# Performance work log

Measured on AMD Instinct MI355X. Metric: run time of the kernel, lower is better.

The kernel has to match this reference:

```python
import jax, jax.numpy as jnp
import numpy as np

N_NODES = 100000
N_EDGES = 1600000
D_IN = 128
D_HID = 128
D_OUT = 1


def setup_inputs() -> dict:
    key = jax.random.key(0)
    ks = jax.random.split(key, 8)
    x = jax.random.normal(ks[0], (N_NODES, D_IN), dtype=jnp.float32)
    edge_index = jax.random.randint(ks[1], (2, N_EDGES), 0, N_NODES, dtype=jnp.int64)
    s1 = 1.0 / np.sqrt(D_IN)
    s2 = 1.0 / np.sqrt(D_HID)
    W1 = jax.random.uniform(ks[2], (D_IN, D_HID), jnp.float32, -s1, s1)
    b1 = jnp.zeros((D_HID,), jnp.float32)
    W2 = jax.random.uniform(ks[3], (D_HID, D_HID), jnp.float32, -s2, s2)
    b2 = jnp.zeros((D_HID,), jnp.float32)
    Wl = jax.random.uniform(ks[4], (D_HID, D_OUT), jnp.float32, -s2, s2)
    bl = jax.random.uniform(ks[5], (D_OUT,), jnp.float32, -s2, s2)
    return {"x": x, "edge_index": edge_index, "W1": W1, "b1": b1,
            "W2": W2, "b2": b2, "Wl": Wl, "bl": bl}


def _gcn_norm(edge_index, num_nodes):
    # Add self-loops, compute symmetric normalization 1/sqrt(deg_s * deg_d).
    loops = jnp.arange(num_nodes, dtype=edge_index.dtype)
    src = jnp.concatenate([edge_index[0], loops])
    dst = jnp.concatenate([edge_index[1], loops])
    deg = jax.ops.segment_sum(jnp.ones_like(dst, dtype=jnp.float32), dst,
                              num_segments=num_nodes)
    dinv = jnp.where(deg > 0, jax.lax.rsqrt(deg), 0.0)
    norm = dinv[src] * dinv[dst]  # [E + N]
    return src, dst, norm


def _gcn_conv(h, W, b, src, dst, norm, num_nodes):
    h = h @ W                                  # [N, d_out]
    msg = h[src] * norm[:, None]               # [E+N, d_out] gather
    out = jax.ops.segment_sum(msg, dst, num_segments=num_nodes)  # scatter-add
    return out + b


def reference(x, edge_index, W1, b1, W2, b2, Wl, bl):
    num_nodes = x.shape[0]
    src, dst, norm = _gcn_norm(edge_index, num_nodes)
    h = jax.nn.relu(_gcn_conv(x, W1, b1, src, dst, norm, num_nodes))
    # dropout is identity in eval mode
    h = jax.nn.relu(_gcn_conv(h, W2, b2, src, dst, norm, num_nodes))
    return h @ Wl + bl
```

## Files before the change

kernel.cpp:

```cpp
#include <hip/hip_runtime.h>

#define DHID 128
#define BCAP 10240
#define PCHUNK 4096
#define XS_LD 136

typedef _Float16 h4 __attribute__((ext_vector_type(4)));
typedef _Float16 h8 __attribute__((ext_vector_type(8)));
typedef _Float16 f16x8 __attribute__((ext_vector_type(8)));
typedef float    f32x4 __attribute__((ext_vector_type(4)));

__global__ __launch_bounds__(256) void k_partition(const int* __restrict__ ei, int E, int nbuck,
                                                   int* __restrict__ bucket_cursor,
                                                   unsigned* __restrict__ packed) {
    __shared__ unsigned sdata[PCHUNK];
    __shared__ int lcnt[256], lbase[256], loff[256], lcur[256], sscan[256];
    int t = threadIdx.x;
    int e0 = blockIdx.x * PCHUNK;
    lcnt[t] = 0;
    __syncthreads();

    int sreg[16], dreg[16];
#pragma unroll
    for (int k = 0; k < 16; ++k) {
        int e = e0 + t + k * 256;
        if (e < E) {
            sreg[k] = ei[e];
            dreg[k] = ei[E + e];
        } else {
            dreg[k] = -1;
        }
    }

#pragma unroll
    for (int k = 0; k < 16; ++k)
        if (dreg[k] >= 0) atomicAdd(&lcnt[dreg[k] >> 9], 1);
    __syncthreads();

    int c = lcnt[t];
    sscan[t] = c;
    __syncthreads();
    for (int off = 1; off < 256; off <<= 1) {
        int v = (t >= off) ? sscan[t - off] : 0;
        __syncthreads();
        sscan[t] += v;
        __syncthreads();
    }
    loff[t] = sscan[t] - c;
    if (t < nbuck && c > 0) lbase[t] = atomicAdd(&bucket_cursor[t], c);
    lcur[t] = sscan[t] - c;
    __syncthreads();

#pragma unroll
    for (int k = 0; k < 16; ++k) {
        if (dreg[k] >= 0) {
            int b = dreg[k] >> 9;
            int pos = atomicAdd(&lcur[b], 1);
            sdata[pos] = ((unsigned)(dreg[k] & 511) << 17) | (unsigned)sreg[k];
        }
    }
    __syncthreads();

    int wid = t >> 6, lane = t & 63;
    for (int b = wid; b < nbuck; b += 4) {
        int cb = lcnt[b];
        if (cb == 0) continue;
        int gbase = b * BCAP + lbase[b];
        int sbase = loff[b];
        for (int k = lane; k < cb; k += 64) packed[gbase + k] = sdata[sbase + k];
    }
}

__global__ void k_bscan(const int* __restrict__ bcur, int* __restrict__ bbase,
                        int* __restrict__ row_ptr, int nbuck, int N, int E) {
    __shared__ int s[256];
    int t = threadIdx.x;
    int c = (t < nbuck) ? bcur[t] : 0;
    s[t] = c;
    __syncthreads();
    for (int off = 1; off < 256; off <<= 1) {
        int v = (t >= off) ? s[t - off] : 0;
        __syncthreads();
        s[t] += v;
        __syncthreads();
    }
    if (t <= nbuck) bbase[t] = (t == 0) ? 0 : s[t - 1];
    if (t == 0) row_ptr[N] = E;
}

__global__ __launch_bounds__(256) void k_p2b(const unsigned* __restrict__ packed,
                                             const int* __restrict__ bucket_cursor,
                                             const int* __restrict__ bbase,
                                             int* __restrict__ row_ptr,
                                             float* __restrict__ dinv,
                                             int* __restrict__ csr, int N) {
    __shared__ int c512[512], cur512[512], sscan[256];
    int t = threadIdx.x, b = blockIdx.x;
    c512[t] = 0; c512[t + 256] = 0;
    __syncthreads();
    int m = bucket_cursor[b];
    const unsigned* pb = packed + (size_t)b * BCAP;
    for (int i = t; i < m; i += 256) atomicAdd(&c512[pb[i] >> 17], 1);
    __syncthreads();
    int v0 = c512[2 * t], v1 = c512[2 * t + 1];
    int ps = v0 + v1;
    sscan[t] = ps;
    __syncthreads();
    for (int off = 1; off < 256; off <<= 1) {
        int v = (t >= off) ? sscan[t - off] : 0;
        __syncthreads();
        sscan[t] += v;
        __syncthreads();
    }
    int excl = sscan[t] - ps;
    cur512[2 * t] = excl;
    cur512[2 * t + 1] = excl + v0;

    int rbase = bbase[b];
    int n0 = (b << 9) + 2 * t;
    if (n0 < N) {
        row_ptr[n0] = rbase + excl;
        dinv[n0] = rsqrtf((float)(v0 + 1));
    }
    if (n0 + 1 < N) {
        row_ptr[n0 + 1] = rbase + excl + v0;
        dinv[n0 + 1] = rsqrtf((float)(v1 + 1));
    }
    __syncthreads();

    for (int i = t; i < m; i += 256) {
        unsigned p = pb[i];
        int dl = p >> 17;
        int src = (int)(p & 0x1FFFFu);
        int pos = atomicAdd(&cur512[dl], 1);
        csr[rbase + pos] = src;
    }
}

template <typename TIN>
__global__ __launch_bounds__(256) void k_gemm_mfma(const TIN* __restrict__ X,
                                                   const float* __restrict__ W,
                                                   const float* __restrict__ dinv,
                                                   _Float16* __restrict__ Th, int N) {
    __shared__ _Float16 Xs[64 * XS_LD];
    int t = threadIdx.x;
    int w = t >> 6;
    int l = t & 63;
    int l16 = l & 15;
    int lq = l >> 4;

    f16x8 afrag[2][4];
#pragma unroll
    for (int ct = 0; ct < 2; ++ct) {
        int c = w * 32 + ct * 16 + l16;
#pragma unroll
        for (int kb = 0; kb < 4; ++kb) {
            f16x8 a;
#pragma unroll
            for (int j = 0; j < 8; ++j)
                a[j] = (_Float16)W[(kb * 32 + lq * 8 + j) * DHID + c];
            afrag[ct][kb] = a;
        }
    }

    int rs = t >> 2;
    int cs = (t & 3) * 32;

    int r0 = blockIdx.x * 64;
    {
        int rg = r0 + rs; if (rg > N - 1) rg = N - 1;
        _Float16* sp = Xs + rs * XS_LD + cs;
        if constexpr (sizeof(TIN) == 4) {
            const float* xp = (const float*)X + (size_t)rg * DHID + cs;
#pragma unroll
            for (int k = 0; k < 4; ++k) {
                float4 a = *(const float4*)(xp + k * 8);
                float4 b = *(const float4*)(xp + k * 8 + 4);
                h8 v;
                v[0] = (_Float16)a.x; v[1] = (_Float16)a.y;
                v[2] = (_Float16)a.z; v[3] = (_Float16)a.w;
                v[4] = (_Float16)b.x; v[5] = (_Float16)b.y;
                v[6] = (_Float16)b.z; v[7] = (_Float16)b.w;
                *(h8*)(sp + k * 8) = v;
            }
        } else {
            const _Float16* xp = (const _Float16*)X + (size_t)rg * DHID + cs;
#pragma unroll
            for (int k = 0; k < 4; ++k)
                *(h8*)(sp + k * 8) = *(const h8*)(xp + k * 8);
        }
    }
    __syncthreads();

    f32x4 acc[4][2];
#pragma unroll
    for (int rt = 0; rt < 4; ++rt)
#pragma unroll
        for (int ct = 0; ct < 2; ++ct) acc[rt][ct] = (f32x4){0.f, 0.f, 0.f, 0.f};

#pragma unroll
    for (int rt = 0; rt < 4; ++rt) {
        const _Float16* bp = Xs + (rt * 16 + l16) * XS_LD + lq * 8;
#pragma unroll
        for (int kb = 0; kb < 4; ++kb) {
            f16x8 b = *(const f16x8*)(bp + kb * 32);
            acc[rt][0] = __builtin_amdgcn_mfma_f32_16x16x32_f16(afrag[0][kb], b, acc[rt][0], 0, 0, 0);
            acc[rt][1] = __builtin_amdgcn_mfma_f32_16x16x32_f16(afrag[1][kb], b, acc[rt][1], 0, 0, 0);
        }
    }

#pragma unroll
    for (int rt = 0; rt < 4; ++rt) {
        int r = r0 + rt * 16 + l16;
        if (r < N) {
            float s = dinv[r];
#pragma unroll
            for (int ct = 0; ct < 2; ++ct) {
                h4 v;
#pragma unroll
                for (int j = 0; j < 4; ++j) v[j] = (_Float16)(acc[rt][ct][j] * s);
                *(h4*)(Th + (size_t)r * DHID + w * 32 + ct * 16 + lq * 4) = v;
            }
        }
    }
}

template <int FINAL>
__global__ __launch_bounds__(256) void k_agg(const _Float16* __restrict__ Th,
                                             const int* __restrict__ row_ptr,
                                             const int* __restrict__ csr_src,
                                             const float* __restrict__ dinv,
                                             const float* __restrict__ bias,
                                             void* __restrict__ outp,
                                             const float* __restrict__ Wl,
                                             const float* __restrict__ bl, int N) {
    int node = blockIdx.x * 16 + (threadIdx.x >> 4);
    int sl = threadIdx.x & 15;
    if (node >= N) return;

    int e = row_ptr[node];
    int end = row_ptr[node + 1];
    const h8* Tl = (const h8*)Th + sl;

    float acc[8];
#pragma unroll
    for (int c = 0; c < 8; ++c) acc[c] = 0.f;

    for (; e + 4 <= end; e += 4) {
        int s0 = csr_src[e];
        int s1 = csr_src[e + 1];
        int s2 = csr_src[e + 2];
        int s3 = csr_src[e + 3];
        h8 v0 = Tl[(size_t)s0 * 16];
        h8 v1 = Tl[(size_t)s1 * 16];
        h8 v2 = Tl[(size_t)s2 * 16];
        h8 v3 = Tl[(size_t)s3 * 16];
#pragma unroll
        for (int c = 0; c < 8; ++c)
            acc[c] += ((float)v0[c] + (float)v1[c]) + ((float)v2[c] + (float)v3[c]);
    }
    for (; e < end; ++e) {
        int s0 = csr_src[e];
        h8 va = Tl[(size_t)s0 * 16];
#pragma unroll
        for (int c = 0; c < 8; ++c) acc[c] += (float)va[c];
    }

    {
        h8 tv = Tl[(size_t)node * 16];
#pragma unroll
        for (int c = 0; c < 8; ++c) acc[c] += (float)tv[c];
    }

    float dn = dinv[node];
    const float* bp = bias + sl * 8;
    float4 b0 = *(const float4*)bp;
    float4 b1 = *(const float4*)(bp + 4);
    float r[8];
    r[0] = fmaxf(fmaf(dn, acc[0], b0.x), 0.f);
    r[1] = fmaxf(fmaf(dn, acc[1], b0.y), 0.f);
    r[2] = fmaxf(fmaf(dn, acc[2], b0.z), 0.f);
    r[3] = fmaxf(fmaf(dn, acc[3], b0.w), 0.f);
    r[4] = fmaxf(fmaf(dn, acc[4], b1.x), 0.f);
    r[5] = fmaxf(fmaf(dn, acc[5], b1.y), 0.f);
    r[6] = fmaxf(fmaf(dn, acc[6], b1.z), 0.f);
    r[7] = fmaxf(fmaf(dn, acc[7], b1.w), 0.f);

    if (FINAL == 0) {
        h8 v;
#pragma unroll
        for (int c = 0; c < 8; ++c) v[c] = (_Float16)r[c];
        *(h8*)((_Float16*)outp + (size_t)node * DHID + sl * 8) = v;
    } else {
        const float* wp = Wl + sl * 8;
        float4 w0 = *(const float4*)wp;
        float4 w1 = *(const float4*)(wp + 4);
        float p = r[0] * w0.x + r[1] * w0.y + r[2] * w0.z + r[3] * w0.w +
                  r[4] * w1.x + r[5] * w1.y + r[6] * w1.z + r[7] * w1.w;
#pragma unroll
        for (int off = 8; off > 0; off >>= 1) p += __shfl_down(p, off, 16);
        if (sl == 0) ((float*)outp)[node] = p + bl[0];
    }
}

extern "C" void kernel_launch(void* const* d_in, const int* in_sizes, int n_in,
                              void* d_out, int out_size, void* d_ws, size_t ws_size,
                              hipStream_t stream) {
    const float* x  = (const float*)d_in[0];
    const int*   ei = (const int*)d_in[1];
    const float* W1 = (const float*)d_in[2];
    const float* b1 = (const float*)d_in[3];
    const float* W2 = (const float*)d_in[4];
    const float* b2 = (const float*)d_in[5];
    const float* Wl = (const float*)d_in[6];
    const float* bl = (const float*)d_in[7];
    float* out = (float*)d_out;

    int N = in_sizes[0] / DHID;
    int E = in_sizes[1] / 2;
    int nbuck = (N + 511) / 512;
    int nRB = (N + 63) / 64;

    char* ws = (char*)d_ws;
    size_t off = 0;
    auto alloc = [&](size_t bytes) -> void* {
        void* p = ws + off;
        off += (bytes + 255) & ~(size_t)255;
        return p;
    };
    float*    dinv     = (float*)alloc((size_t)N * 4);
    int*      row_ptr  = (int*)alloc((size_t)(N + 1) * 4);
    int*      bcur     = (int*)alloc((size_t)nbuck * 4);
    int*      bbase    = (int*)alloc((size_t)(nbuck + 1) * 4);
    int*      csr      = (int*)alloc((size_t)E * 4);
    unsigned* packed   = (unsigned*)alloc((size_t)nbuck * BCAP * 4);
    _Float16* Th       = (_Float16*)alloc((size_t)N * DHID * 2);
    _Float16* H        = (_Float16*)alloc((size_t)N * DHID * 2);

    (void)hipMemsetAsync(bcur, 0, (size_t)nbuck * 4, stream);
    k_partition<<<(E + PCHUNK - 1) / PCHUNK, 256, 0, stream>>>(ei, E, nbuck, bcur, packed);
    k_bscan<<<1, 256, 0, stream>>>(bcur, bbase, row_ptr, nbuck, N, E);
    k_p2b<<<nbuck, 256, 0, stream>>>(packed, bcur, bbase, row_ptr, dinv, csr, N);

    k_gemm_mfma<float><<<nRB, 256, 0, stream>>>(x, W1, dinv, Th, N);
    k_agg<0><<<(N + 15) / 16, 256, 0, stream>>>(Th, row_ptr, csr, dinv, b1, H, nullptr, nullptr, N);

    k_gemm_mfma<_Float16><<<nRB, 256, 0, stream>>>(H, W2, dinv, Th, N);
    k_agg<1><<<(N + 15) / 16, 256, 0, stream>>>(Th, row_ptr, csr, dinv, b2, out, Wl, bl, N);
}
```

Measured before the change: 214.1 us.

## Fuse GEMM1 with edge partition and fuse layer-1 aggregation with GEMM2

Merges the first GEMM and the edge partitioning into one launch by splitting blocks between the two roles. This lets GEMM1 run before the degrees are known, so the per-source dinv scale moves into the aggregation as a gather of dinv[src]. The bucket scan is folded into k_p2b, where every block redoes it. A spare block in that kernel transposes W2 to fp16. Layer-1 aggregation is fused with the GEMM2 MFMA through a 16-row shared tile, which removes the H round trip and two launches, at the cost of an extra dinv gather per edge and a low-row-count MFMA per block.

Measured after the change: 210.4 us. No clear change (-1.8%).

```diff
diff --git a/kernel.cpp b/kernel.cpp
--- a/kernel.cpp
+++ b/kernel.cpp
@@ -4,19 +4,106 @@
 #define BCAP 10240
 #define PCHUNK 4096
 #define XS_LD 136
+#define SMEM_BYTES 21504
 
 typedef _Float16 h4 __attribute__((ext_vector_type(4)));
 typedef _Float16 h8 __attribute__((ext_vector_type(8)));
-typedef _Float16 f16x8 __attribute__((ext_vector_type(8)));
 typedef float    f32x4 __attribute__((ext_vector_type(4)));
 
-__global__ __launch_bounds__(256) void k_partition(const int* __restrict__ ei, int E, int nbuck,
-                                                   int* __restrict__ bucket_cursor,
-                                                   unsigned* __restrict__ packed) {
-    __shared__ unsigned sdata[PCHUNK];
-    __shared__ int lcnt[256], lbase[256], loff[256], lcur[256], sscan[256];
+__device__ inline void hoist_afrag_f16(const _Float16* __restrict__ Wt, int w, int l16, int lq,
+                                       h8 afrag[2][4]) {
+#pragma unroll
+    for (int ct = 0; ct < 2; ++ct) {
+        int c = w * 32 + ct * 16 + l16;
+#pragma unroll
+        for (int kb = 0; kb < 4; ++kb)
+            afrag[ct][kb] = *(const h8*)(Wt + (size_t)c * DHID + kb * 32 + lq * 8);
+    }
+}
+
+__device__ inline void gemm1_body(char* smem, const float* __restrict__ X,
+                                  const float* __restrict__ W,
+                                  _Float16* __restrict__ Th, int N, int blk) {
+    _Float16* Xs = (_Float16*)smem;
     int t = threadIdx.x;
-    int e0 = blockIdx.x * PCHUNK;
+    int w = t >> 6, l = t & 63, l16 = l & 15, lq = l >> 4;
+
+    h8 afrag[2][4];
+#pragma unroll
+    for (int ct = 0; ct < 2; ++ct) {
+        int c = w * 32 + ct * 16 + l16;
+#pragma unroll
+        for (int kb = 0; kb < 4; ++kb) {
+            h8 a;
+#pragma unroll
+            for (int j = 0; j < 8; ++j)
+                a[j] = (_Float16)W[(kb * 32 + lq * 8 + j) * DHID + c];
+            afrag[ct][kb] = a;
+        }
+    }
+
+    int rs = t >> 2, cs = (t & 3) * 32;
+    int r0 = blk * 64;
+    {
+        int rg = r0 + rs; if (rg > N - 1) rg = N - 1;
+        _Float16* sp = Xs + rs * XS_LD + cs;
+        const float* xp = X + (size_t)rg * DHID + cs;
+#pragma unroll
+        for (int k = 0; k < 4; ++k) {
+            float4 a = *(const float4*)(xp + k * 8);
+            float4 b = *(const float4*)(xp + k * 8 + 4);
+            h8 v;
+            v[0] = (_Float16)a.x; v[1] = (_Float16)a.y;
+            v[2] = (_Float16)a.z; v[3] = (_Float16)a.w;
+            v[4] = (_Float16)b.x; v[5] = (_Float16)b.y;
+            v[6] = (_Float16)b.z; v[7] = (_Float16)b.w;
+            *(h8*)(sp + k * 8) = v;
+        }
+    }
+    __syncthreads();
+
+    f32x4 acc[4][2];
+#pragma unroll
+    for (int rt = 0; rt < 4; ++rt)
+#pragma unroll
+        for (int ct = 0; ct < 2; ++ct) acc[rt][ct] = (f32x4){0.f, 0.f, 0.f, 0.f};
+
+#pragma unroll
+    for (int rt = 0; rt < 4; ++rt) {
+        const _Float16* bp = Xs + (rt * 16 + l16) * XS_LD + lq * 8;
+#pragma unroll
+        for (int kb = 0; kb < 4; ++kb) {
+            h8 b = *(const h8*)(bp + kb * 32);
+            acc[rt][0] = __builtin_amdgcn_mfma_f32_16x16x32_f16(afrag[0][kb], b, acc[rt][0], 0, 0, 0);
+            acc[rt][1] = __builtin_amdgcn_mfma_f32_16x16x32_f16(afrag[1][kb], b, acc[rt][1], 0, 0, 0);
+        }
+    }
+
+#pragma unroll
+    for (int rt = 0; rt < 4; ++rt) {
+        int r = r0 + rt * 16 + l16;
+        if (r < N) {
+#pragma unroll
+            for (int ct = 0; ct < 2; ++ct) {
+                h4 v;
+#pragma unroll
+                for (int j = 0; j < 4; ++j) v[j] = (_Float16)acc[rt][ct][j];
+                *(h4*)(Th + (size_t)r * DHID + w * 32 + ct * 16 + lq * 4) = v;
+            }
+        }
+    }
+}
+
+__device__ inline void partition_body(char* smem, const int* __restrict__ ei, int E, int nbuck,
+                                      int* __restrict__ bcur, unsigned* __restrict__ packed, int blk) {
+    unsigned* sdata = (unsigned*)smem;
+    int* lcnt  = (int*)(smem + 16384);
+    int* lbase = (int*)(smem + 17408);
+    int* loff  = (int*)(smem + 18432);
+    int* lcur  = (int*)(smem + 19456);
+    int* sscan = (int*)(smem + 20480);
+    int t = threadIdx.x;
+    int e0 = blk * PCHUNK;
     lcnt[t] = 0;
     __syncthreads();
 
@@ -24,12 +111,8 @@
 #pragma unroll
     for (int k = 0; k < 16; ++k) {
         int e = e0 + t + k * 256;
-        if (e < E) {
-            sreg[k] = ei[e];
-            dreg[k] = ei[E + e];
-        } else {
-            dreg[k] = -1;
-        }
+        if (e < E) { sreg[k] = ei[e]; dreg[k] = ei[E + e]; }
+        else dreg[k] = -1;
     }
 
 #pragma unroll
@@ -47,7 +130,7 @@
         __syncthreads();
     }
     loff[t] = sscan[t] - c;
-    if (t < nbuck && c > 0) lbase[t] = atomicAdd(&bucket_cursor[t], c);
+    if (t < nbuck && c > 0) lbase[t] = atomicAdd(&bcur[t], c);
     lcur[t] = sscan[t] - c;
     __syncthreads();
 
@@ -71,34 +154,52 @@
     }
 }
 
-__global__ void k_bscan(const int* __restrict__ bcur, int* __restrict__ bbase,
-                        int* __restrict__ row_ptr, int nbuck, int N, int E) {
-    __shared__ int s[256];
-    int t = threadIdx.x;
-    int c = (t < nbuck) ? bcur[t] : 0;
-    s[t] = c;
-    __syncthreads();
-    for (int off = 1; off < 256; off <<= 1) {
-        int v = (t >= off) ? s[t - off] : 0;
-        __syncthreads();
-        s[t] += v;
-        __syncthreads();
-    }
-    if (t <= nbuck) bbase[t] = (t == 0) ? 0 : s[t - 1];
-    if (t == 0) row_ptr[N] = E;
+__global__ __launch_bounds__(256) void k_front(const float* __restrict__ X,
+                                               const float* __restrict__ W1,
+                                               _Float16* __restrict__ Th, int N, int nRB,
+                                               const int* __restrict__ ei, int E, int nbuck,
+                                               int* __restrict__ bcur, unsigned* __restrict__ packed) {
+    __shared__ __align__(16) char smem[SMEM_BYTES];
+    if ((int)blockIdx.x < nRB)
+        gemm1_body(smem, X, W1, Th, N, blockIdx.x);
+    else
+        partition_body(smem, ei, E, nbuck, bcur, packed, blockIdx.x - nRB);
 }
 
 __global__ __launch_bounds__(256) void k_p2b(const unsigned* __restrict__ packed,
-                                             const int* __restrict__ bucket_cursor,
-                                             const int* __restrict__ bbase,
+                                             const int* __restrict__ bcur,
                                              int* __restrict__ row_ptr,
                                              float* __restrict__ dinv,
-                                             int* __restrict__ csr, int N) {
-    __shared__ int c512[512], cur512[512], sscan[256];
+                                             int* __restrict__ csr,
+                                             const float* __restrict__ W2,
+                                             _Float16* __restrict__ W2t,
+                                             int nbuck, int N, int E) {
     int t = threadIdx.x, b = blockIdx.x;
+    if (b == nbuck) {
+        int c = t & 127, k0 = (t >> 7) * 64;
+#pragma unroll
+        for (int kb = 0; kb < 8; ++kb) {
+            h8 v;
+#pragma unroll
+            for (int j = 0; j < 8; ++j)
+                v[j] = (_Float16)W2[(size_t)(k0 + kb * 8 + j) * DHID + c];
+            *(h8*)(W2t + (size_t)c * DHID + k0 + kb * 8) = v;
+        }
+        return;
+    }
+
+    __shared__ int c512[512], cur512[512], sscan[256], sbk[256];
+    sbk[t] = (t < nbuck) ? bcur[t] : 0;
     c512[t] = 0; c512[t + 256] = 0;
     __syncthreads();
-    int m = bucket_cursor[b];
+    for (int off = 1; off < 256; off <<= 1) {
+        int v = (t >= off) ? sbk[t - off] : 0;
+        __syncthreads();
+        sbk[t] += v;
+        __syncthreads();
+    }
+    int rbase = (b > 0) ? sbk[b - 1] : 0;
+    int m = bcur[b];
     const unsigned* pb = packed + (size_t)b * BCAP;
     for (int i = t; i < m; i += 256) atomicAdd(&c512[pb[i] >> 17], 1);
     __syncthreads();
@@ -116,7 +217,6 @@
     cur512[2 * t] = excl;
     cur512[2 * t + 1] = excl + v0;
 
-    int rbase = bbase[b];
     int n0 = (b << 9) + 2 * t;
     if (n0 < N) {
         row_ptr[n0] = rbase + excl;
@@ -126,6 +226,7 @@
         row_ptr[n0 + 1] = rbase + excl + v0;
         dinv[n0 + 1] = rsqrtf((float)(v1 + 1));
     }
+    if (b == 0 && t == 0) row_ptr[N] = E;
     __syncthreads();
 
     for (int i = t; i < m; i += 256) {
@@ -137,109 +238,26 @@
     }
 }
 
-template <typename TIN>
-__global__ __launch_bounds__(256) void k_gemm_mfma(const TIN* __restrict__ X,
-                                                   const float* __restrict__ W,
-                                                   const float* __restrict__ dinv,
-                                                   _Float16* __restrict__ Th, int N) {
-    __shared__ _Float16 Xs[64 * XS_LD];
-    int t = threadIdx.x;
-    int w = t >> 6;
-    int l = t & 63;
-    int l16 = l & 15;
-    int lq = l >> 4;
-
-    f16x8 afrag[2][4];
-#pragma unroll
-    for (int ct = 0; ct < 2; ++ct) {
-        int c = w * 32 + ct * 16 + l16;
-#pragma unroll
-        for (int kb = 0; kb < 4; ++kb) {
-            f16x8 a;
-#pragma unroll
-            for (int j = 0; j < 8; ++j)
-                a[j] = (_Float16)W[(kb * 32 + lq * 8 + j) * DHID + c];
-            afrag[ct][kb] = a;
-        }
-    }
-
-    int rs = t >> 2;
-    int cs = (t & 3) * 32;
-
-    int r0 = blockIdx.x * 64;
-    {
-        int rg = r0 + rs; if (rg > N - 1) rg = N - 1;
-        _Float16* sp = Xs + rs * XS_LD + cs;
-        if constexpr (sizeof(TIN) == 4) {
-            const float* xp = (const float*)X + (size_t)rg * DHID + cs;
-#pragma unroll
-            for (int k = 0; k < 4; ++k) {
-                float4 a = *(const float4*)(xp + k * 8);
-                float4 b = *(const float4*)(xp + k * 8 + 4);
-                h8 v;
-                v[0] = (_Float16)a.x; v[1] = (_Float16)a.y;
-                v[2] = (_Float16)a.z; v[3] = (_Float16)a.w;
-                v[4] = (_Float16)b.x; v[5] = (_Float16)b.y;
-                v[6] = (_Float16)b.z; v[7] = (_Float16)b.w;
-                *(h8*)(sp + k * 8) = v;
-            }
-        } else {
-            const _Float16* xp = (const _Float16*)X + (size_t)rg * DHID + cs;
-#pragma unroll
-            for (int k = 0; k < 4; ++k)
-                *(h8*)(sp + k * 8) = *(const h8*)(xp + k * 8);
-        }
-    }
-    __syncthreads();
-
-    f32x4 acc[4][2];
-#pragma unroll
-    for (int rt = 0; rt < 4; ++rt)
-#pragma unroll
-        for (int ct = 0; ct < 2; ++ct) acc[rt][ct] = (f32x4){0.f, 0.f, 0.f, 0.f};
-
-#pragma unroll
-    for (int rt = 0; rt < 4; ++rt) {
-        const _Float16* bp = Xs + (rt * 16 + l16) * XS_LD + lq * 8;
-#pragma unroll
-        for (int kb = 0; kb < 4; ++kb) {
-            f16x8 b = *(const f16x8*)(bp + kb * 32);
-            acc[rt][0] = __builtin_amdgcn_mfma_f32_16x16x32_f16(afrag[0][kb], b, acc[rt][0], 0, 0, 0);
-            acc[rt][1] = __builtin_amdgcn_mfma_f32_16x16x32_f16(afrag[1][kb], b, acc[rt][1], 0, 0, 0);
-        }
-    }
-
-#pragma unroll
-    for (int rt = 0; rt < 4; ++rt) {
-        int r = r0 + rt * 16 + l16;
-        if (r < N) {
-            float s = dinv[r];
-#pragma unroll
-            for (int ct = 0; ct < 2; ++ct) {
-                h4 v;
-#pragma unroll
-                for (int j = 0; j < 4; ++j) v[j] = (_Float16)(acc[rt][ct][j] * s);
-                *(h4*)(Th + (size_t)r * DHID + w * 32 + ct * 16 + lq * 4) = v;
-            }
-        }
-    }
-}
-
-template <int FINAL>
-__global__ __launch_bounds__(256) void k_agg(const _Float16* __restrict__ Th,
-                                             const int* __restrict__ row_ptr,
-                                             const int* __restrict__ csr_src,
-                                             const float* __restrict__ dinv,
-                                             const float* __restrict__ bias,
-                                             void* __restrict__ outp,
-                                             const float* __restrict__ Wl,
-                                             const float* __restrict__ bl, int N) {
-    int node = blockIdx.x * 16 + (threadIdx.x >> 4);
-    int sl = threadIdx.x & 15;
-    if (node >= N) return;
-
-    int e = row_ptr[node];
-    int end = row_ptr[node + 1];
+__global__ __launch_bounds__(256) void k_agg_gemm(const _Float16* __restrict__ Th,
+                                                  const int* __restrict__ row_ptr,
+                                                  const int* __restrict__ csr,
+                                                  const float* __restrict__ dinv,
+                                                  const float* __restrict__ bias,
+                                                  const _Float16* __restrict__ W2t,
+                                                  _Float16* __restrict__ Th2, int N) {
+    __shared__ _Float16 Hs[16 * XS_LD];
+    int t = threadIdx.x, w = t >> 6, l = t & 63, l16 = l & 15, lq = l >> 4;
+
+    h8 afrag[2][4];
+    hoist_afrag_f16(W2t, w, l16, lq, afrag);
+
+    int g = t >> 4, sl = t & 15;
+    int node = blockIdx.x * 16 + g;
+    bool valid = node < N;
+    int nc = valid ? node : N - 1;
+    int e = row_ptr[nc];
+    int end = row_ptr[nc + 1];
+    if (!valid) end = e;
     const h8* Tl = (const h8*)Th + sl;
 
     float acc[8];
@@ -247,32 +265,117 @@
     for (int c = 0; c < 8; ++c) acc[c] = 0.f;
 
     for (; e + 4 <= end; e += 4) {
-        int s0 = csr_src[e];
-        int s1 = csr_src[e + 1];
-        int s2 = csr_src[e + 2];
-        int s3 = csr_src[e + 3];
+        int s0 = csr[e], s1 = csr[e + 1], s2 = csr[e + 2], s3 = csr[e + 3];
+        float d0 = dinv[s0], d1 = dinv[s1], d2 = dinv[s2], d3 = dinv[s3];
         h8 v0 = Tl[(size_t)s0 * 16];
         h8 v1 = Tl[(size_t)s1 * 16];
         h8 v2 = Tl[(size_t)s2 * 16];
         h8 v3 = Tl[(size_t)s3 * 16];
 #pragma unroll
-        for (int c = 0; c < 8; ++c)
-            acc[c] += ((float)v0[c] + (float)v1[c]) + ((float)v2[c] + (float)v3[c]);
+        for (int c = 0; c < 8; ++c) {
+            float a0 = fmaf(d0, (float)v0[c], fmaf(d1, (float)v1[c], 0.f));
+            float a1 = fmaf(d2, (float)v2[c], fmaf(d3, (float)v3[c], 0.f));
+            acc[c] += a0 + a1;
+        }
     }
     for (; e < end; ++e) {
-        int s0 = csr_src[e];
+        int s0 = csr[e];
+        float d0 = dinv[s0];
         h8 va = Tl[(size_t)s0 * 16];
 #pragma unroll
-        for (int c = 0; c < 8; ++c) acc[c] += (float)va[c];
-    }
-
+        for (int c = 0; c < 8; ++c) acc[c] = fmaf(d0, (float)va[c], acc[c]);
+    }
+
+    float dn = valid ? dinv[nc] : 0.f;
+    {
+        h8 tv = Tl[(size_t)nc * 16];
+#pragma unroll
+        for (int c = 0; c < 8; ++c) acc[c] = fmaf(dn, (float)tv[c], acc[c]);
+    }
+
+    const float* bp = bias + sl * 8;
+    float4 b0 = *(const float4*)bp;
+    float4 b1 = *(const float4*)(bp + 4);
+    h8 hv;
+    hv[0] = (_Float16)fmaxf(fmaf(dn, acc[0], b0.x), 0.f);
+    hv[1] = (_Float16)fmaxf(fmaf(dn, acc[1], b0.y), 0.f);
+    hv[2] = (_Float16)fmaxf(fmaf(dn, acc[2], b0.z), 0.f);
+    hv[3] = (_Float16)fmaxf(fmaf(dn, acc[3], b0.w), 0.f);
+    hv[4] = (_Float16)fmaxf(fmaf(dn, acc[4], b1.x), 0.f);
+    hv[5] = (_Float16)fmaxf(fmaf(dn, acc[5], b1.y), 0.f);
+    hv[6] = (_Float16)fmaxf(fmaf(dn, acc[6], b1.z), 0.f);
+    hv[7] = (_Float16)fmaxf(fmaf(dn, acc[7], b1.w), 0.f);
+    *(h8*)(Hs + g * XS_LD + sl * 8) = hv;
+    __syncthreads();
+
+    f32x4 am[2] = {(f32x4){0.f, 0.f, 0.f, 0.f}, (f32x4){0.f, 0.f, 0.f, 0.f}};
+#pragma unroll
+    for (int kb = 0; kb < 4; ++kb) {
+        h8 bfr = *(const h8*)(Hs + l16 * XS_LD + kb * 32 + lq * 8);
+        am[0] = __builtin_amdgcn_mfma_f32_16x16x32_f16(afrag[0][kb], bfr, am[0], 0, 0, 0);
+        am[1] = __builtin_amdgcn_mfma_f32_16x16x32_f16(afrag[1][kb], bfr, am[1], 0, 0, 0);
+    }
+    int rg = blockIdx.x * 16 + l16;
+    if (rg < N) {
+#pragma unroll
+        for (int ct = 0; ct < 2; ++ct) {
+            h4 v;
+#pragma unroll
+            for (int j = 0; j < 4; ++j) v[j] = (_Float16)am[ct][j];
+            *(h4*)(Th2 + (size_t)rg * DHID + w * 32 + ct * 16 + lq * 4) = v;
+        }
+    }
+}
+
+__global__ __launch_bounds__(256) void k_agg_fin(const _Float16* __restrict__ Th2,
+                                                 const int* __restrict__ row_ptr,
+                                                 const int* __restrict__ csr,
+                                                 const float* __restrict__ dinv,
+                                                 const float* __restrict__ bias,
+                                                 const float* __restrict__ Wl,
+                                                 const float* __restrict__ bl,
+                                                 float* __restrict__ out, int N) {
+    int node = blockIdx.x * 16 + (threadIdx.x >> 4);
+    int sl = threadIdx.x & 15;
+    if (node >= N) return;
+
+    int e = row_ptr[node];
+    int end = row_ptr[node + 1];
+    const h8* Tl = (const h8*)Th2 + sl;
+
+    float acc[8];
+#pragma unroll
+    for (int c = 0; c < 8; ++c) acc[c] = 0.f;
+
+    for (; e + 4 <= end; e += 4) {
+        int s0 = csr[e], s1 = csr[e + 1], s2 = csr[e + 2], s3 = csr[e + 3];
+        float d0 = dinv[s0], d1 = dinv[s1], d2 = dinv[s2], d3 = dinv[s3];
+        h8 v0 = Tl[(size_t)s0 * 16];
+        h8 v1 = Tl[(size_t)s1 * 16];
+        h8 v2 = Tl[(size_t)s2 * 16];
+        h8 v3 = Tl[(size_t)s3 * 16];
+#pragma unroll
+        for (int c = 0; c < 8; ++c) {
+            float a0 = fmaf(d0, (float)v0[c], fmaf(d1, (float)v1[c], 0.f));
+            float a1 = fmaf(d2, (float)v2[c], fmaf(d3, (float)v3[c], 0.f));
+            acc[c] += a0 + a1;
+        }
+    }
+    for (; e < end; ++e) {
+        int s0 = csr[e];
+        float d0 = dinv[s0];
+        h8 va = Tl[(size_t)s0 * 16];
+#pragma unroll
+        for (int c = 0; c < 8; ++c) acc[c] = fmaf(d0, (float)va[c], acc[c]);
+    }
+
+    float dn = dinv[node];
     {
         h8 tv = Tl[(size_t)node * 16];
 #pragma unroll
-        for (int c = 0; c < 8; ++c) acc[c] += (float)tv[c];
-    }
-
-    float dn = dinv[node];
+        for (int c = 0; c < 8; ++c) acc[c] = fmaf(dn, (float)tv[c], acc[c]);
+    }
+
     const float* bp = bias + sl * 8;
     float4 b0 = *(const float4*)bp;
     float4 b1 = *(const float4*)(bp + 4);
@@ -286,21 +389,14 @@
     r[6] = fmaxf(fmaf(dn, acc[6], b1.z), 0.f);
     r[7] = fmaxf(fmaf(dn, acc[7], b1.w), 0.f);
 
-    if (FINAL == 0) {
-        h8 v;
-#pragma unroll
-        for (int c = 0; c < 8; ++c) v[c] = (_Float16)r[c];
-        *(h8*)((_Float16*)outp + (size_t)node * DHID + sl * 8) = v;
-    } else {
-        const float* wp = Wl + sl * 8;
-        float4 w0 = *(const float4*)wp;
-        float4 w1 = *(const float4*)(wp + 4);
-        float p = r[0] * w0.x + r[1] * w0.y + r[2] * w0.z + r[3] * w0.w +
-                  r[4] * w1.x + r[5] * w1.y + r[6] * w1.z + r[7] * w1.w;
-#pragma unroll
-        for (int off = 8; off > 0; off >>= 1) p += __shfl_down(p, off, 16);
-        if (sl == 0) ((float*)outp)[node] = p + bl[0];
-    }
+    const float* wp = Wl + sl * 8;
+    float4 w0 = *(const float4*)wp;
+    float4 w1 = *(const float4*)(wp + 4);
+    float p = r[0] * w0.x + r[1] * w0.y + r[2] * w0.z + r[3] * w0.w +
+              r[4] * w1.x + r[5] * w1.y + r[6] * w1.z + r[7] * w1.w;
+#pragma unroll
+    for (int off = 8; off > 0; off >>= 1) p += __shfl_down(p, off, 16);
+    if (sl == 0) out[node] = p + bl[0];
 }
 
 extern "C" void kernel_launch(void* const* d_in, const int* in_sizes, int n_in,
@@ -320,6 +416,7 @@
     int E = in_sizes[1] / 2;
     int nbuck = (N + 511) / 512;
     int nRB = (N + 63) / 64;
+    int nPart = (E + PCHUNK - 1) / PCHUNK;
 
     char* ws = (char*)d_ws;
     size_t off = 0;
@@ -331,20 +428,16 @@
     float*    dinv     = (float*)alloc((size_t)N * 4);
     int*      row_ptr  = (int*)alloc((size_t)(N + 1) * 4);
     int*      bcur     = (int*)alloc((size_t)nbuck * 4);
-    int*      bbase    = (int*)alloc((size_t)(nbuck + 1) * 4);
     int*      csr      = (int*)alloc((size_t)E * 4);
     unsigned* packed   = (unsigned*)alloc((size_t)nbuck * BCAP * 4);
     _Float16* Th       = (_Float16*)alloc((size_t)N * DHID * 2);
-    _Float16* H        = (_Float16*)alloc((size_t)N * DHID * 2);
+    _Float16* Th2      = (_Float16*)alloc((size_t)N * DHID * 2);
+    _Float16* W2t      = (_Float16*)alloc((size_t)DHID * DHID * 2);
 
     (void)hipMemsetAsync(bcur, 0, (size_t)nbuck * 4, stream);
-    k_partition<<<(E + PCHUNK - 1) / PCHUNK, 256, 0, stream>>>(ei, E, nbuck, bcur, packed);
-    k_bscan<<<1, 256, 0, stream>>>(bcur, bbase, row_ptr, nbuck, N, E);
-    k_p2b<<<nbuck, 256, 0, stream>>>(packed, bcur, bbase, row_ptr, dinv, csr, N);
-
-    k_gemm_mfma<float><<<nRB, 256, 0, stream>>>(x, W1, dinv, Th, N);
-    k_agg<0><<<(N + 15) / 16, 256, 0, stream>>>(Th, row_ptr, csr, dinv, b1, H, nullptr, nullptr, N);
-
-    k_gemm_mfma<_Float16><<<nRB, 256, 0, stream>>>(H, W2, dinv, Th, N);
-    k_agg<1><<<(N + 15) / 16, 256, 0, stream>>>(Th, row_ptr, csr, dinv, b2, out, Wl, bl, N);
-}
+
+    k_front<<<nRB + nPart, 256, 0, stream>>>(x, W1, Th, N, nRB, ei, E, nbuck, bcur, packed);
+    k_p2b<<<nbuck + 1, 256, 0, stream>>>(packed, bcur, row_ptr, dinv, csr, W2, W2t, nbuck, N, E);
+    k_agg_gemm<<<(N + 15) / 16, 256, 0, stream>>>(Th, row_ptr, csr, dinv, b1, W2t, Th2, N);
+    k_agg_fin<<<(N + 15) / 16, 256, 0, stream>>>(Th2, row_ptr, csr, dinv, b2, Wl, bl, out, N);
+}
```
